# Performance work log

Hardware: AMD Instinct MI355X
Metric: run time of the kernel (lower is better)

The kernel has to match this reference:

```python
import jax, jax.numpy as jnp
import numpy as np

B, T = 64, 2048
DEC, ENC, ATT, LOC, K = 1024, 512, 128, 32, 31


def setup_inputs() -> dict:
    key = jax.random.key(0)
    ks = jax.random.split(key, 9)
    inv = lambda n: 1.0 / np.sqrt(n)
    return {
        "query": jax.random.normal(ks[0], (B, DEC), dtype=jnp.float32),
        "values": jax.random.normal(ks[1], (B, T, ENC), dtype=jnp.float32),
        "cumulative_attention_weights": jax.random.uniform(ks[2], (B, T), dtype=jnp.float32),
        "mask": jnp.zeros((B, T), dtype=bool),
        "Q_w": jax.random.uniform(ks[3], (ATT, DEC), jnp.float32, -inv(DEC), inv(DEC)),
        "Q_b": jax.random.uniform(ks[4], (ATT,), jnp.float32, -inv(DEC), inv(DEC)),
        "V_w": jax.random.uniform(ks[5], (ATT, ENC), jnp.float32, -inv(ENC), inv(ENC)),
        "conv_w": jax.random.uniform(ks[6], (LOC, 1, K), jnp.float32, -inv(K), inv(K)),
        "loc_proj_w": jax.random.uniform(ks[7], (ATT, LOC), jnp.float32, -inv(LOC), inv(LOC)),
        "v_w": jax.random.uniform(ks[8], (1, ATT), jnp.float32, -inv(ATT), inv(ATT)),
    }


def reference(query, values, cumulative_attention_weights, mask,
              Q_w, Q_b, V_w, conv_w, loc_proj_w, v_w):
    # query projection: [B, 1, ATT] (broadcast over T)
    q = query @ Q_w.T + Q_b                       # [B, ATT]
    q = q[:, None, :]
    # values cache: [B, T, ATT]
    v_cache = jnp.einsum("bte,ae->bta", values, V_w)
    # location features: Conv1d(1 -> LOC, k=31, same padding) over cum weights
    x = cumulative_attention_weights[:, None, :]   # [B, 1, T]
    loc = jax.lax.conv_general_dilated(
        x, conv_w, window_strides=(1,), padding="SAME",
        dimension_numbers=("NCH", "OIH", "NCH"))   # [B, LOC, T]
    loc = jnp.einsum("bct,ac->bta", loc, loc_proj_w)  # [B, T, ATT]
    # additive attention energies
    energies = jnp.tanh(q + v_cache + loc) @ v_w[0]   # [B, T]
    energies = jnp.where(mask, -jnp.inf, energies)
    attention_weights = jax.nn.softmax(energies, axis=1)
    # context: [B, ENC]
    attention_context = jnp.einsum("bt,bte->be", attention_weights, values)
    return attention_context, attention_weights
```

## Files before the change

kernel.cpp:

```cpp
#include <hip/hip_runtime.h>
#include <hip/hip_bf16.h>
#include <math.h>

#define B_  64
#define T_  2048
#define DEC_ 1024
#define ENC_ 512
#define ATT_ 128
#define LOC_ 32
#define KW_  31

typedef __attribute__((ext_vector_type(8))) short short8;
typedef __attribute__((ext_vector_type(4))) float f32x4;

__device__ inline unsigned short bf16_rn(float x) {
    unsigned int u = __builtin_bit_cast(unsigned int, x);
    unsigned int r = u + 0x7fffu + ((u >> 16) & 1u);
    return (unsigned short)(r >> 16);
}
__device__ inline float bf16_to_f(unsigned short h) {
    unsigned int u = ((unsigned int)h) << 16;
    return __builtin_bit_cast(float, u);
}

__global__ __launch_bounds__(256) void prep_kernel(
    const float* __restrict__ query, const float* __restrict__ Q_w,
    const float* __restrict__ Q_b, const float* __restrict__ conv_w,
    const float* __restrict__ loc_proj_w, const float* __restrict__ V_w,
    float* __restrict__ qbuf,
    unsigned short* __restrict__ Bph, unsigned short* __restrict__ Bpl,
    unsigned short* __restrict__ effh, unsigned short* __restrict__ effl)
{
    int bi = blockIdx.x, tid = threadIdx.x;
    if (bi < B_) {
        __shared__ float sq[DEC_];
        *(float4*)(&sq[tid * 4]) = *(const float4*)(query + bi * DEC_ + tid * 4);
        __syncthreads();
        int w = tid >> 6, lane = tid & 63;
        for (int a = w * 32; a < w * 32 + 32; a += 2) {
            const float* r0 = Q_w + (size_t)a * DEC_;
            const float* r1 = r0 + DEC_;
            float s0 = 0.f, s1 = 0.f;
            #pragma unroll
            for (int i = 0; i < 4; ++i) {
                float4 q0 = *(const float4*)(r0 + i * 256 + lane * 4);
                float4 q1 = *(const float4*)(r1 + i * 256 + lane * 4);
                float4 xq = *(const float4*)(sq + i * 256 + lane * 4);
                s0 += q0.x * xq.x + q0.y * xq.y + q0.z * xq.z + q0.w * xq.w;
                s1 += q1.x * xq.x + q1.y * xq.y + q1.z * xq.z + q1.w * xq.w;
            }
            #pragma unroll
            for (int m = 32; m >= 1; m >>= 1) {
                s0 += __shfl_xor(s0, m, 64);
                s1 += __shfl_xor(s1, m, 64);
            }
            if (lane == 0) {
                qbuf[bi * ATT_ + a]     = s0 + Q_b[a];
                qbuf[bi * ATT_ + a + 1] = s1 + Q_b[a + 1];
            }
        }
    } else if (bi == B_) {
        __shared__ float slp[ATT_ * LOC_];
        __shared__ float scw[LOC_ * KW_];
        for (int i = tid; i < ATT_ * LOC_; i += 256) slp[i] = loc_proj_w[i];
        for (int i = tid; i < LOC_ * KW_; i += 256) scw[i] = conv_w[i];
        __syncthreads();
        if (tid < ATT_) {
            int n = tid;
            for (int k = 0; k < 32; ++k) {
                float s = 0.f;
                if (k < KW_)
                    #pragma unroll
                    for (int c = 0; c < LOC_; ++c)
                        s += slp[n * LOC_ + c] * scw[c * KW_ + k];
                unsigned short h = bf16_rn(s);
                effh[n * 32 + k] = h;
                effl[n * 32 + k] = bf16_rn(s - bf16_to_f(h));
            }
        }
    } else {
        int g0 = (bi - B_ - 1) * 512;
        #pragma unroll
        for (int p = 0; p < 2; ++p) {
            int gi = g0 + p * 256 + tid;
            int n  = gi >> 7;
            int kq = (gi & 127) * 4;
            float4 v = ((const float4*)V_w)[gi];
            ushort4 h4, l4;
            h4.x = bf16_rn(v.x); l4.x = bf16_rn(v.x - bf16_to_f(h4.x));
            h4.y = bf16_rn(v.y); l4.y = bf16_rn(v.y - bf16_to_f(h4.y));
            h4.z = bf16_rn(v.z); l4.z = bf16_rn(v.z - bf16_to_f(h4.z));
            h4.w = bf16_rn(v.w); l4.w = bf16_rn(v.w - bf16_to_f(h4.w));
            int dst = (kq >> 5) * 4096 + n * 32 + (kq & 31);
            *(ushort4*)(Bph + dst) = h4;
            *(ushort4*)(Bpl + dst) = l4;
        }
    }
}

#define KC 64
#define LDA 72

__global__ __launch_bounds__(256, 3) void energy_kernel(
    const float* __restrict__ values, const float* __restrict__ cum,
    const float* __restrict__ qbuf,
    const unsigned short* __restrict__ Bph, const unsigned short* __restrict__ Bpl,
    const unsigned short* __restrict__ effh, const unsigned short* __restrict__ effl,
    const float* __restrict__ vw, float* __restrict__ energies)
{
    __shared__ unsigned short sAh[128 * LDA];
    __shared__ unsigned short sAl[128 * LDA];
    __shared__ float sx[160];
    __shared__ float sred[256];

    const int tid = threadIdx.x;
    const int bx  = blockIdx.x;
    const int b   = bx >> 4;
    const int t0  = (bx & 15) * 128;

    if (tid < 158) {
        int g = t0 - 15 + tid;
        sx[tid] = (g >= 0 && g < T_) ? cum[b * T_ + g] : 0.f;
    }

    const int w      = tid >> 6;
    const int lane   = tid & 63;
    const int lane15 = lane & 15;
    const int quad   = lane >> 4;
    const int wm0    = (w & 1) * 64;
    const int wn0    = (w >> 1) * 64;

    f32x4 acc[4][4];
    #pragma unroll
    for (int i = 0; i < 4; ++i)
        #pragma unroll
        for (int j = 0; j < 4; ++j) acc[i][j] = (f32x4){0.f, 0.f, 0.f, 0.f};

    const float* aptr = values + ((size_t)b * T_ + t0) * ENC_;
    const int ar = tid >> 4;
    const int ac = (tid & 15) * 4;

    float4 pf[8];
    #pragma unroll
    for (int p = 0; p < 8; ++p)
        pf[p] = *(const float4*)(aptr + (size_t)(p * 16 + ar) * ENC_ + ac);

    for (int kc = 0; kc < ENC_; kc += KC) {
        __syncthreads();
        #pragma unroll
        for (int p = 0; p < 8; ++p) {
            int r = p * 16 + ar;
            float4 v = pf[p];
            ushort4 h4, l4;
            h4.x = bf16_rn(v.x); l4.x = bf16_rn(v.x - bf16_to_f(h4.x));
            h4.y = bf16_rn(v.y); l4.y = bf16_rn(v.y - bf16_to_f(h4.y));
            h4.z = bf16_rn(v.z); l4.z = bf16_rn(v.z - bf16_to_f(h4.z));
            h4.w = bf16_rn(v.w); l4.w = bf16_rn(v.w - bf16_to_f(h4.w));
            *(ushort4*)(&sAh[r * LDA + ac]) = h4;
            *(ushort4*)(&sAl[r * LDA + ac]) = l4;
        }
        __syncthreads();
        if (kc + KC < ENC_) {
            #pragma unroll
            for (int p = 0; p < 8; ++p)
                pf[p] = *(const float4*)(aptr + (size_t)(p * 16 + ar) * ENC_ + kc + KC + ac);
        }
        #pragma unroll
        for (int ks = 0; ks < KC; ks += 32) {
            const int base  = ks + quad * 8;
            const int chunk = ((kc + ks) >> 5) * 4096;
            short8 ah[4], al[4];
            #pragma unroll
            for (int i = 0; i < 4; ++i) {
                int row = (wm0 + i * 16 + lane15) * LDA + base;
                ah[i] = *(const short8*)(&sAh[row]);
                al[i] = *(const short8*)(&sAl[row]);
            }
            #pragma unroll
            for (int j = 0; j < 4; ++j) {
                int n = wn0 + j * 16 + lane15;
                short8 bh = *(const short8*)(Bph + chunk + n * 32 + quad * 8);
                short8 bl = *(const short8*)(Bpl + chunk + n * 32 + quad * 8);
                #pragma unroll
                for (int i = 0; i < 4; ++i) {
                    acc[i][j] = __builtin_amdgcn_mfma_f32_16x16x32_bf16(ah[i], bh, acc[i][j], 0, 0, 0);
                    acc[i][j] = __builtin_amdgcn_mfma_f32_16x16x32_bf16(ah[i], bl, acc[i][j], 0, 0, 0);
                    acc[i][j] = __builtin_amdgcn_mfma_f32_16x16x32_bf16(al[i], bh, acc[i][j], 0, 0, 0);
                }
            }
        }
    }

    __syncthreads();
    #pragma unroll
    for (int p = 0; p < 16; ++p) {
        int idx = p * 256 + tid;
        int r = idx >> 5, k = idx & 31;
        float xv = (k < KW_) ? sx[r + k] : 0.f;
        unsigned short h = bf16_rn(xv);
        sAh[r * LDA + k] = h;
        sAl[r * LDA + k] = bf16_rn(xv - bf16_to_f(h));
    }
    __syncthreads();
    {
        const int base = quad * 8;
        short8 ah[4], al[4];
        #pragma unroll
        for (int i = 0; i < 4; ++i) {
            int row = (wm0 + i * 16 + lane15) * LDA + base;
            ah[i] = *(const short8*)(&sAh[row]);
            al[i] = *(const short8*)(&sAl[row]);
        }
        #pragma unroll
        for (int j = 0; j < 4; ++j) {
            int n = wn0 + j * 16 + lane15;
            short8 bh = *(const short8*)(effh + n * 32 + base);
            short8 bl = *(const short8*)(effl + n * 32 + base);
            #pragma unroll
            for (int i = 0; i < 4; ++i) {
                acc[i][j] = __builtin_amdgcn_mfma_f32_16x16x32_bf16(ah[i], bh, acc[i][j], 0, 0, 0);
                acc[i][j] = __builtin_amdgcn_mfma_f32_16x16x32_bf16(ah[i], bl, acc[i][j], 0, 0, 0);
                acc[i][j] = __builtin_amdgcn_mfma_f32_16x16x32_bf16(al[i], bh, acc[i][j], 0, 0, 0);
            }
        }
    }

    float qv[4], vv[4];
    #pragma unroll
    for (int j = 0; j < 4; ++j) {
        int n = wn0 + j * 16 + lane15;
        qv[j] = qbuf[b * ATT_ + n];
        vv[j] = vw[n];
    }
    #pragma unroll
    for (int i = 0; i < 4; ++i) {
        #pragma unroll
        for (int reg = 0; reg < 4; ++reg) {
            float s = 0.f;
            #pragma unroll
            for (int j = 0; j < 4; ++j) {
                float z = acc[i][j][reg] + qv[j];
                s += vv[j] * tanhf(z);
            }
            #pragma unroll
            for (int m = 8; m >= 1; m >>= 1) s += __shfl_xor(s, m, 64);
            if (lane15 == 0)
                sred[(w >> 1) * 128 + wm0 + i * 16 + quad * 4 + reg] = s;
        }
    }
    __syncthreads();
    if (tid < 128)
        energies[b * T_ + t0 + tid] = sred[tid] + sred[128 + tid];
}

__global__ __launch_bounds__(256) void softmax_kernel(
    const float* __restrict__ energies, const unsigned char* __restrict__ mask,
    float* __restrict__ out)
{
    int b = blockIdx.x, tid = threadIdx.x;
    float* ctx  = out;
    float* wout = out + B_ * ENC_;

    for (int i = tid; i < ENC_; i += 256) ctx[b * ENC_ + i] = 0.f;

    float e[8];
    float mx = -INFINITY;
    #pragma unroll
    for (int p = 0; p < 8; ++p) {
        int t = p * 256 + tid;
        float v = energies[b * T_ + t];
        if (mask[b * T_ + t]) v = -INFINITY;
        e[p] = v;
        mx = fmaxf(mx, v);
    }
    #pragma unroll
    for (int m = 32; m >= 1; m >>= 1) mx = fmaxf(mx, __shfl_xor(mx, m, 64));
    __shared__ float red[8];
    int wave = tid >> 6;
    if ((tid & 63) == 0) red[wave] = mx;
    __syncthreads();
    mx = fmaxf(fmaxf(red[0], red[1]), fmaxf(red[2], red[3]));

    float sum = 0.f;
    #pragma unroll
    for (int p = 0; p < 8; ++p) {
        e[p] = expf(e[p] - mx);
        sum += e[p];
    }
    #pragma unroll
    for (int m = 32; m >= 1; m >>= 1) sum += __shfl_xor(sum, m, 64);
    if ((tid & 63) == 0) red[4 + wave] = sum;
    __syncthreads();
    sum = red[4] + red[5] + red[6] + red[7];
    float inv = 1.f / sum;
    #pragma unroll
    for (int p = 0; p < 8; ++p)
        wout[b * T_ + p * 256 + tid] = e[p] * inv;
}

__global__ __launch_bounds__(256) void context_kernel(
    const float* __restrict__ values, const float* __restrict__ w,
    float* __restrict__ ctx)
{
    int bx = blockIdx.x;
    int b = bx >> 4, seg = bx & 15;
    int tid = threadIdx.x;
    int tt = tid >> 7;
    int e4 = (tid & 127) * 4;

    __shared__ float sw[128];
    if (tid < 128) sw[tid] = w[b * T_ + seg * 128 + tid];
    __syncthreads();

    const float* vp = values + ((size_t)b * T_ + seg * 128) * ENC_ + e4;
    float4 acc = make_float4(0.f, 0.f, 0.f, 0.f);
    #pragma unroll 8
    for (int t = 0; t < 64; ++t) {
        int tg = tt * 64 + t;
        float4 v = *(const float4*)(vp + (size_t)tg * ENC_);
        float wv = sw[tg];
        acc.x += wv * v.x; acc.y += wv * v.y;
        acc.z += wv * v.z; acc.w += wv * v.w;
    }

    __shared__ float red[512];
    if (tt == 1) *(float4*)&red[e4] = acc;
    __syncthreads();
    if (tt == 0) {
        float4 o = *(const float4*)&red[e4];
        atomicAdd(&ctx[b * ENC_ + e4 + 0], acc.x + o.x);
        atomicAdd(&ctx[b * ENC_ + e4 + 1], acc.y + o.y);
        atomicAdd(&ctx[b * ENC_ + e4 + 2], acc.z + o.z);
        atomicAdd(&ctx[b * ENC_ + e4 + 3], acc.w + o.w);
    }
}

extern "C" void kernel_launch(void* const* d_in, const int* in_sizes, int n_in,
                              void* d_out, int out_size, void* d_ws, size_t ws_size,
                              hipStream_t stream) {
    const float* query        = (const float*)d_in[0];
    const float* values       = (const float*)d_in[1];
    const float* cum          = (const float*)d_in[2];
    const unsigned char* mask = (const unsigned char*)d_in[3];
    const float* Q_w          = (const float*)d_in[4];
    const float* Q_b          = (const float*)d_in[5];
    const float* V_w          = (const float*)d_in[6];
    const float* conv_w       = (const float*)d_in[7];
    const float* loc_proj_w   = (const float*)d_in[8];
    const float* v_w          = (const float*)d_in[9];

    float* out = (float*)d_out;
    char*  ws  = (char*)d_ws;
    float*          qbuf     = (float*)(ws);
    float*          energies = (float*)(ws + 32768);
    unsigned short* Bph      = (unsigned short*)(ws + 557056);
    unsigned short* Bpl      = (unsigned short*)(ws + 688128);
    unsigned short* effh     = (unsigned short*)(ws + 819200);
    unsigned short* effl     = (unsigned short*)(ws + 827392);

    prep_kernel<<<97, 256, 0, stream>>>(query, Q_w, Q_b, conv_w, loc_proj_w, V_w,
                                        qbuf, Bph, Bpl, effh, effl);
    energy_kernel<<<1024, 256, 0, stream>>>(values, cum, qbuf, Bph, Bpl,
                                            effh, effl, v_w, energies);
    softmax_kernel<<<B_, 256, 0, stream>>>(energies, mask, out);
    context_kernel<<<B_ * 16, 256, 0, stream>>>(values, out + B_ * ENC_, out);
}
```

Before: 493.2 us.

## Load values directly into MFMA registers, drop LDS staging in energy kernel

The energy kernel no longer stages the values tile in shared memory. Each wave now owns 32 rows and all 128 attention columns, loads its float values straight from global memory into MFMA A-fragments, and converts them to split bf16 in registers, which removes the LDS stores and barriers and the cross-wave energy reduction. The prep kernel spreads the query projection over 256 blocks instead of 64, and the context kernel uses twice as many blocks over shorter time segments. The cost is more accumulator registers per wave (occupancy hint lowered to 2) and global loads whose per-lane access is less coalesced.

```diff
diff --git a/kernel.cpp b/kernel.cpp
--- a/kernel.cpp
+++ b/kernel.cpp
@@ -21,6 +21,15 @@
 __device__ inline float bf16_to_f(unsigned short h) {
     unsigned int u = ((unsigned int)h) << 16;
     return __builtin_bit_cast(float, u);
+}
+__device__ inline void cvt_pair(float4 a, float4 b2, short8& hi, short8& lo) {
+    float f[8] = {a.x, a.y, a.z, a.w, b2.x, b2.y, b2.z, b2.w};
+    #pragma unroll
+    for (int j = 0; j < 8; ++j) {
+        unsigned short h = bf16_rn(f[j]);
+        hi[j] = (short)h;
+        lo[j] = (short)bf16_rn(f[j] - bf16_to_f(h));
+    }
 }
 
 __global__ __launch_bounds__(256) void prep_kernel(
@@ -32,12 +41,15 @@
     unsigned short* __restrict__ effh, unsigned short* __restrict__ effl)
 {
     int bi = blockIdx.x, tid = threadIdx.x;
-    if (bi < B_) {
+    if (bi < 256) {
+        int b = bi >> 2, grp = bi & 3;
         __shared__ float sq[DEC_];
-        *(float4*)(&sq[tid * 4]) = *(const float4*)(query + bi * DEC_ + tid * 4);
+        *(float4*)(&sq[tid * 4]) = *(const float4*)(query + (size_t)b * DEC_ + tid * 4);
         __syncthreads();
         int w = tid >> 6, lane = tid & 63;
-        for (int a = w * 32; a < w * 32 + 32; a += 2) {
+        int a0 = grp * 32 + w * 8;
+        for (int p = 0; p < 4; ++p) {
+            int a = a0 + 2 * p;
             const float* r0 = Q_w + (size_t)a * DEC_;
             const float* r1 = r0 + DEC_;
             float s0 = 0.f, s1 = 0.f;
@@ -55,11 +67,11 @@
                 s1 += __shfl_xor(s1, m, 64);
             }
             if (lane == 0) {
-                qbuf[bi * ATT_ + a]     = s0 + Q_b[a];
-                qbuf[bi * ATT_ + a + 1] = s1 + Q_b[a + 1];
-            }
-        }
-    } else if (bi == B_) {
+                qbuf[b * ATT_ + a]     = s0 + Q_b[a];
+                qbuf[b * ATT_ + a + 1] = s1 + Q_b[a + 1];
+            }
+        }
+    } else if (bi == 256) {
         __shared__ float slp[ATT_ * LOC_];
         __shared__ float scw[LOC_ * KW_];
         for (int i = tid; i < ATT_ * LOC_; i += 256) slp[i] = loc_proj_w[i];
@@ -79,7 +91,7 @@
             }
         }
     } else {
-        int g0 = (bi - B_ - 1) * 512;
+        int g0 = (bi - 257) * 512;
         #pragma unroll
         for (int p = 0; p < 2; ++p) {
             int gi = g0 + p * 256 + tid;
@@ -98,126 +110,99 @@
     }
 }
 
-#define KC 64
-#define LDA 72
-
-__global__ __launch_bounds__(256, 3) void energy_kernel(
+__global__ __launch_bounds__(256, 2) void energy_kernel(
     const float* __restrict__ values, const float* __restrict__ cum,
     const float* __restrict__ qbuf,
     const unsigned short* __restrict__ Bph, const unsigned short* __restrict__ Bpl,
     const unsigned short* __restrict__ effh, const unsigned short* __restrict__ effl,
     const float* __restrict__ vw, float* __restrict__ energies)
 {
-    __shared__ unsigned short sAh[128 * LDA];
-    __shared__ unsigned short sAl[128 * LDA];
     __shared__ float sx[160];
-    __shared__ float sred[256];
 
     const int tid = threadIdx.x;
     const int bx  = blockIdx.x;
     const int b   = bx >> 4;
     const int t0  = (bx & 15) * 128;
 
-    if (tid < 158) {
+    if (tid < 160) {
         int g = t0 - 15 + tid;
         sx[tid] = (g >= 0 && g < T_) ? cum[b * T_ + g] : 0.f;
     }
+    __syncthreads();
 
     const int w      = tid >> 6;
     const int lane   = tid & 63;
     const int lane15 = lane & 15;
     const int quad   = lane >> 4;
-    const int wm0    = (w & 1) * 64;
-    const int wn0    = (w >> 1) * 64;
-
-    f32x4 acc[4][4];
-    #pragma unroll
-    for (int i = 0; i < 4; ++i)
-        #pragma unroll
-        for (int j = 0; j < 4; ++j) acc[i][j] = (f32x4){0.f, 0.f, 0.f, 0.f};
-
-    const float* aptr = values + ((size_t)b * T_ + t0) * ENC_;
-    const int ar = tid >> 4;
-    const int ac = (tid & 15) * 4;
-
-    float4 pf[8];
-    #pragma unroll
-    for (int p = 0; p < 8; ++p)
-        pf[p] = *(const float4*)(aptr + (size_t)(p * 16 + ar) * ENC_ + ac);
-
-    for (int kc = 0; kc < ENC_; kc += KC) {
-        __syncthreads();
-        #pragma unroll
-        for (int p = 0; p < 8; ++p) {
-            int r = p * 16 + ar;
-            float4 v = pf[p];
-            ushort4 h4, l4;
-            h4.x = bf16_rn(v.x); l4.x = bf16_rn(v.x - bf16_to_f(h4.x));
-            h4.y = bf16_rn(v.y); l4.y = bf16_rn(v.y - bf16_to_f(h4.y));
-            h4.z = bf16_rn(v.z); l4.z = bf16_rn(v.z - bf16_to_f(h4.z));
-            h4.w = bf16_rn(v.w); l4.w = bf16_rn(v.w - bf16_to_f(h4.w));
-            *(ushort4*)(&sAh[r * LDA + ac]) = h4;
-            *(ushort4*)(&sAl[r * LDA + ac]) = l4;
-        }
-        __syncthreads();
-        if (kc + KC < ENC_) {
-            #pragma unroll
-            for (int p = 0; p < 8; ++p)
-                pf[p] = *(const float4*)(aptr + (size_t)(p * 16 + ar) * ENC_ + kc + KC + ac);
-        }
-        #pragma unroll
-        for (int ks = 0; ks < KC; ks += 32) {
-            const int base  = ks + quad * 8;
-            const int chunk = ((kc + ks) >> 5) * 4096;
-            short8 ah[4], al[4];
-            #pragma unroll
-            for (int i = 0; i < 4; ++i) {
-                int row = (wm0 + i * 16 + lane15) * LDA + base;
-                ah[i] = *(const short8*)(&sAh[row]);
-                al[i] = *(const short8*)(&sAl[row]);
-            }
-            #pragma unroll
-            for (int j = 0; j < 4; ++j) {
-                int n = wn0 + j * 16 + lane15;
-                short8 bh = *(const short8*)(Bph + chunk + n * 32 + quad * 8);
-                short8 bl = *(const short8*)(Bpl + chunk + n * 32 + quad * 8);
-                #pragma unroll
-                for (int i = 0; i < 4; ++i) {
-                    acc[i][j] = __builtin_amdgcn_mfma_f32_16x16x32_bf16(ah[i], bh, acc[i][j], 0, 0, 0);
-                    acc[i][j] = __builtin_amdgcn_mfma_f32_16x16x32_bf16(ah[i], bl, acc[i][j], 0, 0, 0);
-                    acc[i][j] = __builtin_amdgcn_mfma_f32_16x16x32_bf16(al[i], bh, acc[i][j], 0, 0, 0);
-                }
-            }
-        }
-    }
-
-    __syncthreads();
-    #pragma unroll
-    for (int p = 0; p < 16; ++p) {
-        int idx = p * 256 + tid;
-        int r = idx >> 5, k = idx & 31;
-        float xv = (k < KW_) ? sx[r + k] : 0.f;
-        unsigned short h = bf16_rn(xv);
-        sAh[r * LDA + k] = h;
-        sAl[r * LDA + k] = bf16_rn(xv - bf16_to_f(h));
-    }
-    __syncthreads();
+
+    f32x4 acc[2][8];
+    #pragma unroll
+    for (int i = 0; i < 2; ++i)
+        #pragma unroll
+        for (int j = 0; j < 8; ++j) acc[i][j] = (f32x4){0.f, 0.f, 0.f, 0.f};
+
+    const float* abase = values + ((size_t)b * T_ + t0 + w * 32 + lane15) * ENC_ + quad * 8;
+    const unsigned short* bbh = Bph + lane15 * 32 + quad * 8;
+    const unsigned short* bbl = Bpl + lane15 * 32 + quad * 8;
+
+    float4 pf[2][2];
+    #pragma unroll
+    for (int i = 0; i < 2; ++i) {
+        pf[i][0] = *(const float4*)(abase + i * 16 * ENC_);
+        pf[i][1] = *(const float4*)(abase + i * 16 * ENC_ + 4);
+    }
+
+    for (int kc = 0; kc < ENC_; kc += 32) {
+        short8 ah[2], al[2];
+        #pragma unroll
+        for (int i = 0; i < 2; ++i) cvt_pair(pf[i][0], pf[i][1], ah[i], al[i]);
+
+        short8 bh[8], bl[8];
+        const int chunk = (kc >> 5) * 4096;
+        #pragma unroll
+        for (int j = 0; j < 8; ++j) {
+            bh[j] = *(const short8*)(bbh + chunk + j * 512);
+            bl[j] = *(const short8*)(bbl + chunk + j * 512);
+        }
+        __builtin_amdgcn_sched_barrier(0);
+        if (kc + 32 < ENC_) {
+            #pragma unroll
+            for (int i = 0; i < 2; ++i) {
+                pf[i][0] = *(const float4*)(abase + i * 16 * ENC_ + kc + 32);
+                pf[i][1] = *(const float4*)(abase + i * 16 * ENC_ + kc + 36);
+            }
+        }
+        __builtin_amdgcn_sched_barrier(0);
+        #pragma unroll
+        for (int j = 0; j < 8; ++j)
+            #pragma unroll
+            for (int i = 0; i < 2; ++i) {
+                acc[i][j] = __builtin_amdgcn_mfma_f32_16x16x32_bf16(ah[i], bh[j], acc[i][j], 0, 0, 0);
+                acc[i][j] = __builtin_amdgcn_mfma_f32_16x16x32_bf16(ah[i], bl[j], acc[i][j], 0, 0, 0);
+                acc[i][j] = __builtin_amdgcn_mfma_f32_16x16x32_bf16(al[i], bh[j], acc[i][j], 0, 0, 0);
+            }
+    }
+
     {
-        const int base = quad * 8;
-        short8 ah[4], al[4];
-        #pragma unroll
-        for (int i = 0; i < 4; ++i) {
-            int row = (wm0 + i * 16 + lane15) * LDA + base;
-            ah[i] = *(const short8*)(&sAh[row]);
-            al[i] = *(const short8*)(&sAl[row]);
-        }
-        #pragma unroll
-        for (int j = 0; j < 4; ++j) {
-            int n = wn0 + j * 16 + lane15;
-            short8 bh = *(const short8*)(effh + n * 32 + base);
-            short8 bl = *(const short8*)(effl + n * 32 + base);
-            #pragma unroll
-            for (int i = 0; i < 4; ++i) {
+        short8 ah[2], al[2];
+        #pragma unroll
+        for (int i = 0; i < 2; ++i) {
+            int base = w * 32 + i * 16 + lane15 + quad * 8;
+            #pragma unroll
+            for (int j2 = 0; j2 < 8; ++j2) {
+                float xv = sx[base + j2];
+                unsigned short h = bf16_rn(xv);
+                ah[i][j2] = (short)h;
+                al[i][j2] = (short)bf16_rn(xv - bf16_to_f(h));
+            }
+        }
+        #pragma unroll
+        for (int j = 0; j < 8; ++j) {
+            int n = j * 16 + lane15;
+            short8 bh = *(const short8*)(effh + n * 32 + quad * 8);
+            short8 bl = *(const short8*)(effl + n * 32 + quad * 8);
+            #pragma unroll
+            for (int i = 0; i < 2; ++i) {
                 acc[i][j] = __builtin_amdgcn_mfma_f32_16x16x32_bf16(ah[i], bh, acc[i][j], 0, 0, 0);
                 acc[i][j] = __builtin_amdgcn_mfma_f32_16x16x32_bf16(ah[i], bl, acc[i][j], 0, 0, 0);
                 acc[i][j] = __builtin_amdgcn_mfma_f32_16x16x32_bf16(al[i], bh, acc[i][j], 0, 0, 0);
@@ -225,32 +210,26 @@
         }
     }
 
-    float qv[4], vv[4];
-    #pragma unroll
-    for (int j = 0; j < 4; ++j) {
-        int n = wn0 + j * 16 + lane15;
+    float qv[8], vv[8];
+    #pragma unroll
+    for (int j = 0; j < 8; ++j) {
+        int n = j * 16 + lane15;
         qv[j] = qbuf[b * ATT_ + n];
         vv[j] = vw[n];
     }
     #pragma unroll
-    for (int i = 0; i < 4; ++i) {
-        #pragma unroll
-        for (int reg = 0; reg < 4; ++reg) {
+    for (int i = 0; i < 2; ++i)
+        #pragma unroll
+        for (int r = 0; r < 4; ++r) {
             float s = 0.f;
             #pragma unroll
-            for (int j = 0; j < 4; ++j) {
-                float z = acc[i][j][reg] + qv[j];
-                s += vv[j] * tanhf(z);
-            }
+            for (int j = 0; j < 8; ++j)
+                s += vv[j] * tanhf(acc[i][j][r] + qv[j]);
             #pragma unroll
             for (int m = 8; m >= 1; m >>= 1) s += __shfl_xor(s, m, 64);
             if (lane15 == 0)
-                sred[(w >> 1) * 128 + wm0 + i * 16 + quad * 4 + reg] = s;
-        }
-    }
-    __syncthreads();
-    if (tid < 128)
-        energies[b * T_ + t0 + tid] = sred[tid] + sred[128 + tid];
+                energies[b * T_ + t0 + w * 32 + i * 16 + quad * 4 + r] = s;
+        }
 }
 
 __global__ __launch_bounds__(256) void softmax_kernel(
@@ -303,22 +282,21 @@
     float* __restrict__ ctx)
 {
     int bx = blockIdx.x;
-    int b = bx >> 4, seg = bx & 15;
+    int b = bx >> 5, seg = bx & 31;
     int tid = threadIdx.x;
     int tt = tid >> 7;
     int e4 = (tid & 127) * 4;
 
-    __shared__ float sw[128];
-    if (tid < 128) sw[tid] = w[b * T_ + seg * 128 + tid];
-    __syncthreads();
-
-    const float* vp = values + ((size_t)b * T_ + seg * 128) * ENC_ + e4;
+    __shared__ float sw[64];
+    if (tid < 64) sw[tid] = w[b * T_ + seg * 64 + tid];
+    __syncthreads();
+
+    const float* vp = values + ((size_t)b * T_ + seg * 64) * ENC_ + e4;
     float4 acc = make_float4(0.f, 0.f, 0.f, 0.f);
     #pragma unroll 8
-    for (int t = 0; t < 64; ++t) {
-        int tg = tt * 64 + t;
-        float4 v = *(const float4*)(vp + (size_t)tg * ENC_);
-        float wv = sw[tg];
+    for (int t = tt * 32; t < tt * 32 + 32; ++t) {
+        float4 v = *(const float4*)(vp + (size_t)t * ENC_);
+        float wv = sw[t];
         acc.x += wv * v.x; acc.y += wv * v.y;
         acc.z += wv * v.z; acc.w += wv * v.w;
     }
@@ -352,16 +330,16 @@
     float* out = (float*)d_out;
     char*  ws  = (char*)d_ws;
     float*          qbuf     = (float*)(ws);
-    float*          energies = (float*)(ws + 32768);
-    unsigned short* Bph      = (unsigned short*)(ws + 557056);
-    unsigned short* Bpl      = (unsigned short*)(ws + 688128);
-    unsigned short* effh     = (unsigned short*)(ws + 819200);
-    unsigned short* effl     = (unsigned short*)(ws + 827392);
-
-    prep_kernel<<<97, 256, 0, stream>>>(query, Q_w, Q_b, conv_w, loc_proj_w, V_w,
-                                        qbuf, Bph, Bpl, effh, effl);
+    unsigned short* Bph      = (unsigned short*)(ws + 32768);
+    unsigned short* Bpl      = (unsigned short*)(ws + 163840);
+    unsigned short* effh     = (unsigned short*)(ws + 294912);
+    unsigned short* effl     = (unsigned short*)(ws + 303104);
+    float*          energies = (float*)(ws + 311296);
+
+    prep_kernel<<<289, 256, 0, stream>>>(query, Q_w, Q_b, conv_w, loc_proj_w, V_w,
+                                         qbuf, Bph, Bpl, effh, effl);
     energy_kernel<<<1024, 256, 0, stream>>>(values, cum, qbuf, Bph, Bpl,
                                             effh, effl, v_w, energies);
     softmax_kernel<<<B_, 256, 0, stream>>>(energies, mask, out);
-    context_kernel<<<B_ * 16, 256, 0, stream>>>(values, out + B_ * ENC_, out);
-}
+    context_kernel<<<B_ * 32, 256, 0, stream>>>(values, out + B_ * ENC_, out);
+}
```

Result: faster. 479.8 us (-2.7%).
